# Kernel tuning notes

Measured on AMD Instinct MI355X. Metric: run time of the kernel, lower is better.

The kernel has to match this reference:

```python
import jax, jax.numpy as jnp
import numpy as np

EPS = 1e-8           # torch.cosine_similarity norm clamp
TEMPERATURE = 0.2    # from __init__ default


def setup_inputs() -> dict:
    key = jax.random.key(0)
    k1, k2, k3 = jax.random.split(key, 3)
    B, C, D = 16384, 1000, 2048  # batch, num_classes, embedding_size
    querys = jax.random.normal(k1, (B, D), dtype=jnp.float32)
    prototype = jax.random.normal(k2, (C, D), dtype=jnp.float32)
    fc_w = jax.random.normal(k3, (C, D), dtype=jnp.float32) * 0.02
    fc_b = jnp.zeros((C,), dtype=jnp.float32)
    return {"querys": querys, "prototype": prototype, "fc_w": fc_w, "fc_b": fc_b}


def _memory_prototype_attention(querys, prototype):
    # cosine similarity of every query against every prototype, fused as one GEMM
    qn = jnp.maximum(jnp.linalg.norm(querys, axis=1, keepdims=True), EPS)      # [B,1]
    pn = jnp.maximum(jnp.linalg.norm(prototype, axis=1, keepdims=True), EPS)   # [C,1]
    cos = jnp.einsum('bd,cd->bc', querys / qn, prototype / pn)                 # [B,C]
    attn = jax.nn.softmax(cos / TEMPERATURE, axis=1)                           # [B,C]
    enhanced = jnp.einsum('bc,cd->bd', attn, prototype)                        # [B,D]
    # original skips rows where the raw score sum is exactly zero
    nonzero = (jnp.sum(cos, axis=1, keepdims=True) != 0)
    return jnp.where(nonzero, enhanced, jnp.zeros_like(enhanced))


def reference(querys, prototype, fc_w, fc_b):
    embedding = querys  # post-avgpool features in the original forward
    enhanced = jax.lax.stop_gradient(_memory_prototype_attention(querys, prototype))
    x = querys + enhanced
    logits = x @ fc_w.T + fc_b  # [B, num_classes]
    return (logits, embedding)
```

## Files before the change

### kernel.cpp

```cpp
#include <hip/hip_runtime.h>
#include <hip/hip_bf16.h>
#include <cstdint>
#include <math.h>

typedef __attribute__((ext_vector_type(8))) __bf16 bfx8;
typedef __attribute__((ext_vector_type(4))) __bf16 bfx4;
typedef __attribute__((ext_vector_type(4))) float f32x4;

#define EPSN 1e-8f
#define SM_SCALE 7.2134752044448170f

__device__ __forceinline__ void gload_lds16(const void* g, void* l) {
    __builtin_amdgcn_global_load_lds(
        (__attribute__((address_space(1))) void*)g,
        (__attribute__((address_space(3))) void*)l,
        16, 0, 0);
}

__global__ __launch_bounds__(256) void qnorm_kernel(
    const float* __restrict__ q, __bf16* __restrict__ qbf,
    float* __restrict__ emb, int D) {
    const int tid = threadIdx.x;
    const size_t roff = (size_t)blockIdx.x * D;
    const float4* qr = (const float4*)(q + roff);
    float4* er = (float4*)(emb + roff);
    const int PASS = D >> 10;
    float4 v[4];
    float ss = 0.f;
    for (int p = 0; p < PASS; ++p) {
        v[p] = qr[p * 256 + tid];
        ss += v[p].x * v[p].x + v[p].y * v[p].y + v[p].z * v[p].z + v[p].w * v[p].w;
    }
    for (int o = 32; o; o >>= 1) ss += __shfl_xor(ss, o);
    __shared__ float sred[4];
    if ((tid & 63) == 0) sred[tid >> 6] = ss;
    __syncthreads();
    float tot = sred[0] + sred[1] + sred[2] + sred[3];
    float inv = 1.f / fmaxf(sqrtf(tot), EPSN);
    for (int p = 0; p < PASS; ++p) {
        er[p * 256 + tid] = v[p];
        bfx4 o4 = {(__bf16)(v[p].x * inv), (__bf16)(v[p].y * inv),
                   (__bf16)(v[p].z * inv), (__bf16)(v[p].w * inv)};
        *(bfx4*)(qbf + roff + (size_t)(p * 256 + tid) * 4) = o4;
    }
}

__global__ __launch_bounds__(256) void pnorm_kernel(
    const float* __restrict__ P, const float* __restrict__ W,
    __bf16* __restrict__ Pn, __bf16* __restrict__ Wb,
    int C, int D) {
    const int c = blockIdx.x;
    const int tid = threadIdx.x;
    const int PASS = D >> 10;
    if (c >= C) {
        bfx4 z = {(__bf16)0.f, (__bf16)0.f, (__bf16)0.f, (__bf16)0.f};
        for (int p = 0; p < PASS; ++p) {
            size_t e = (size_t)c * D + (size_t)(p * 256 + tid) * 4;
            *(bfx4*)(Pn + e) = z;
            *(bfx4*)(Wb + e) = z;
        }
        return;
    }
    const float4* pr = (const float4*)(P + (size_t)c * D);
    float4 v[4];
    float ss = 0.f;
    for (int p = 0; p < PASS; ++p) {
        v[p] = pr[p * 256 + tid];
        ss += v[p].x * v[p].x + v[p].y * v[p].y + v[p].z * v[p].z + v[p].w * v[p].w;
    }
    for (int o = 32; o; o >>= 1) ss += __shfl_xor(ss, o);
    __shared__ float sred[4];
    if ((tid & 63) == 0) sred[tid >> 6] = ss;
    __syncthreads();
    float tot = sred[0] + sred[1] + sred[2] + sred[3];
    float inv = 1.f / fmaxf(sqrtf(tot), EPSN);
    const float4* wr_ = (const float4*)(W + (size_t)c * D);
    for (int p = 0; p < PASS; ++p) {
        size_t e = (size_t)c * D + (size_t)(p * 256 + tid) * 4;
        bfx4 o4 = {(__bf16)(v[p].x * inv), (__bf16)(v[p].y * inv),
                   (__bf16)(v[p].z * inv), (__bf16)(v[p].w * inv)};
        *(bfx4*)(Pn + e) = o4;
        float4 wv = wr_[p * 256 + tid];
        bfx4 w4 = {(__bf16)wv.x, (__bf16)wv.y, (__bf16)wv.z, (__bf16)wv.w};
        *(bfx4*)(Wb + e) = w4;
    }
}

__global__ __launch_bounds__(256) void ptrans_kernel(
    const float* __restrict__ P, __bf16* __restrict__ PT,
    int C, int D, int CP) {
    __shared__ float t[64][65];
    const int d0 = blockIdx.x * 64;
    const int c0 = blockIdx.y * 64;
    const int tid = threadIdx.x;
#pragma unroll
    for (int it = 0; it < 16; ++it) {
        int idx = it * 256 + tid;
        int r = idx >> 6;
        int cc = idx & 63;
        float v = 0.f;
        if (c0 + r < C) v = P[(size_t)(c0 + r) * D + d0 + cc];
        t[r][cc] = v;
    }
    __syncthreads();
#pragma unroll
    for (int it = 0; it < 16; ++it) {
        int idx = it * 256 + tid;
        int dd = idx >> 6;
        int c = idx & 63;
        PT[(size_t)(d0 + dd) * CP + c0 + c] = (__bf16)t[c][dd];
    }
}

__global__ __launch_bounds__(256) void softmax_kernel(
    __bf16* __restrict__ S, int C, int CP) {
    const int tid = threadIdx.x;
    __bf16* row = S + (size_t)blockIdx.x * CP;
    bfx4 v4 = *(const bfx4*)(row + tid * 4);
    const int base = tid * 4;
    float v[4];
    float mx = -INFINITY, rs = 0.f;
#pragma unroll
    for (int j = 0; j < 4; ++j) {
        v[j] = (float)v4[j];
        if (base + j < C) { mx = fmaxf(mx, v[j]); rs += v[j]; }
    }
    for (int o = 32; o; o >>= 1) {
        mx = fmaxf(mx, __shfl_xor(mx, o));
        rs += __shfl_xor(rs, o);
    }
    __shared__ float smx[4], srs[4], sps[4];
    if ((tid & 63) == 0) { smx[tid >> 6] = mx; srs[tid >> 6] = rs; }
    __syncthreads();
    mx = fmaxf(fmaxf(smx[0], smx[1]), fmaxf(smx[2], smx[3]));
    rs = srs[0] + srs[1] + srs[2] + srs[3];
    float p[4], ps = 0.f;
#pragma unroll
    for (int j = 0; j < 4; ++j) {
        p[j] = (base + j < C) ? exp2f((v[j] - mx) * SM_SCALE) : 0.f;
        ps += p[j];
    }
    for (int o = 32; o; o >>= 1) ps += __shfl_xor(ps, o);
    if ((tid & 63) == 0) sps[tid >> 6] = ps;
    __syncthreads();
    ps = sps[0] + sps[1] + sps[2] + sps[3];
    float inv = (rs != 0.f) ? 1.f / ps : 0.f;
    bfx4 o4 = {(__bf16)(p[0] * inv), (__bf16)(p[1] * inv),
               (__bf16)(p[2] * inv), (__bf16)(p[3] * inv)};
    *(bfx4*)(row + tid * 4) = o4;
}

template <int MODE>
__global__ __launch_bounds__(512, 2) void gemm8p(
    const __bf16* __restrict__ A, const __bf16* __restrict__ B_,
    int K, int NT, int nbxl, int nwg,
    void* __restrict__ out, const float* __restrict__ aux, int ldout) {
    __shared__ __bf16 lds[65536];

    const int tid = threadIdx.x;
    const int lane = tid & 63, wid = tid >> 6;
    const int wr = wid >> 2, wc = wid & 3;
    const int fr = lane & 15, fq = lane >> 4;
    const int wr4 = wr * 4, wc2 = wc * 2;
    const int frs = fr * 32 + ((fq * 8) ^ ((fr & 8) << 1));

    const int nbx = 1 << nbxl;
    const int lin = blockIdx.y * nbx + blockIdx.x;
    const int swz = (lin & 7) * (nwg >> 3) + (lin >> 3);
    const int bm0 = (swz >> nbxl) * 256;
    const int bn0 = (swz & (nbx - 1)) * 256;

    int row0, col0, row1, col1;
    {
        int Le = tid * 8;
        int st = Le >> 9, w = Le & 511;
        row0 = (st >> 1) * 16 + (w >> 5);
        col0 = (st & 1) * 32 + ((w & 31) ^ ((w >> 4) & 16));
        Le = tid * 8 + 4096;
        st = Le >> 9; w = Le & 511;
        row1 = (st >> 1) * 16 + (w >> 5);
        col1 = (st & 1) * 32 + ((w & 31) ^ ((w >> 4) & 16));
    }
    const __bf16* Ap = A + (size_t)bm0 * K;
    const __bf16* Bp = B_ + (size_t)bn0 * K;
    const size_t hstride = (size_t)128 * K;
    const __bf16* srcA0 = Ap + (size_t)row0 * K + col0;
    const __bf16* srcA1 = Ap + (size_t)row1 * K + col1;
    const __bf16* srcB0 = Bp + (size_t)row0 * K + col0;
    const __bf16* srcB1 = Bp + (size_t)row1 * K + col1;
    const int ldsoff = tid * 8;

#define STG(H, t) do {                                                         \
    const int kt_ = (t) << 6;                                                  \
    __bf16* d_ = lds + ((((t) & 1) << 14) + (((H) >> 1) << 13) +               \
                        (((H) & 1) ? 32768 : 0)) + ldsoff;                     \
    const __bf16* s0_ = (((H) & 1) ? srcB0 : srcA0) +                          \
                        (((H) >> 1) ? hstride : 0) + kt_;                      \
    const __bf16* s1_ = (((H) & 1) ? srcB1 : srcA1) +                          \
                        (((H) >> 1) ? hstride : 0) + kt_;                      \
    gload_lds16(s0_, d_);                                                      \
    gload_lds16(s1_, d_ + 4096);                                               \
} while (0)

    bfx8 fA0[4][2], fA1[4][2], fB0[2][2], fB1[2][2];
    f32x4 acc[4][4][2] = {};

#define RDA(F, H, BUFE) do {                                                   \
    _Pragma("unroll") for (int m_ = 0; m_ < 4; ++m_)                           \
      _Pragma("unroll") for (int ks_ = 0; ks_ < 2; ++ks_)                      \
        F[m_][ks_] = *(const bfx8*)&lds[(BUFE) +                               \
            (((((H) * 8) + wr4 + m_) * 2 + ks_) << 9) + frs];                  \
} while (0)
#define RDB(F, H, BUFE) do {                                                   \
    _Pragma("unroll") for (int n_ = 0; n_ < 2; ++n_)                           \
      _Pragma("unroll") for (int ks_ = 0; ks_ < 2; ++ks_)                      \
        F[n_][ks_] = *(const bfx8*)&lds[32768 + (BUFE) +                       \
            (((((H) * 8) + wc2 + n_) * 2 + ks_) << 9) + frs];                  \
} while (0)
#define MM(QI, FA, FB) do {                                                    \
    __builtin_amdgcn_s_setprio(1);                                             \
    _Pragma("unroll") for (int ks_ = 0; ks_ < 2; ++ks_)                        \
      _Pragma("unroll") for (int m_ = 0; m_ < 4; ++m_)                         \
        _Pragma("unroll") for (int n_ = 0; n_ < 2; ++n_)                       \
          acc[QI][m_][n_] = __builtin_amdgcn_mfma_f32_16x16x32_bf16(           \
              FA[m_][ks_], FB[n_][ks_], acc[QI][m_][n_], 0, 0, 0);             \
    __builtin_amdgcn_s_setprio(0);                                             \
} while (0)
#define BAR __builtin_amdgcn_s_barrier()
#define LGKM(N) asm volatile("s_waitcnt lgkmcnt(" #N ")" ::: "memory")
#define VMC(N) asm volatile("s_waitcnt vmcnt(" #N ")" ::: "memory")

    STG(0, 0); STG(1, 0); STG(2, 0); STG(3, 0);
    STG(0, 1); STG(1, 1);
    VMC(4);
    BAR;
    RDA(fA0, 0, 0);
    RDB(fB0, 0, 0);

    for (int T = 0; T <= NT - 3; ++T) {
        const int bufe = (T & 1) << 14, nbufe = bufe ^ 16384;
        RDB(fB1, 1, bufe); STG(2, T + 1); BAR; LGKM(4);
        MM(0, fA0, fB0); BAR;
        RDA(fA1, 1, bufe); STG(3, T + 1); BAR; LGKM(8);
        MM(1, fA0, fB1); BAR;
        STG(0, T + 2); BAR; LGKM(0);
        MM(3, fA1, fB1); BAR;
        STG(1, T + 2); BAR;
        MM(2, fA1, fB0); VMC(4); BAR;
        RDA(fA0, 0, nbufe); RDB(fB0, 0, nbufe);
    }
    {
        const int T = NT - 2;
        const int bufe = (T & 1) << 14, nbufe = bufe ^ 16384;
        RDB(fB1, 1, bufe); STG(2, T + 1); BAR; LGKM(4);
        MM(0, fA0, fB0); BAR;
        RDA(fA1, 1, bufe); STG(3, T + 1); BAR; LGKM(8);
        MM(1, fA0, fB1); BAR;
        BAR; LGKM(0);
        MM(3, fA1, fB1); BAR;
        BAR;
        MM(2, fA1, fB0); VMC(0); BAR;
        RDA(fA0, 0, nbufe); RDB(fB0, 0, nbufe);
    }
    {
        const int bufe = ((NT - 1) & 1) << 14;
        RDB(fB1, 1, bufe); BAR; LGKM(4);
        MM(0, fA0, fB0); BAR;
        RDA(fA1, 1, bufe); BAR; LGKM(8);
        MM(1, fA0, fB1); BAR;
        BAR; LGKM(0);
        MM(3, fA1, fB1); BAR;
        MM(2, fA1, fB0);
    }
#undef STG
#undef RDA
#undef RDB
#undef MM
#undef BAR
#undef LGKM
#undef VMC

#pragma unroll
    for (int q = 0; q < 4; ++q) {
        const int qm_ = q >> 1, qn_ = q & 1;
#pragma unroll
        for (int m = 0; m < 4; ++m) {
            const int grb = bm0 + qm_ * 128 + wr * 64 + m * 16 + fq * 4;
#pragma unroll
            for (int n = 0; n < 2; ++n) {
                const int gc = bn0 + qn_ * 128 + wc * 32 + n * 16 + fr;
#pragma unroll
                for (int j = 0; j < 4; ++j) {
                    const int gr = grb + j;
                    const float va = acc[q][m][n][j];
                    if (MODE == 0) {
                        ((__bf16*)out)[(size_t)gr * ldout + gc] = (__bf16)va;
                    } else if (MODE == 1) {
                        ((__bf16*)out)[(size_t)gr * ldout + gc] =
                            (__bf16)(va + aux[(size_t)gr * ldout + gc]);
                    } else {
                        if (gc < ldout)
                            ((float*)out)[(size_t)gr * ldout + gc] = va + aux[gc];
                    }
                }
            }
        }
    }
}

extern "C" void kernel_launch(void* const* d_in, const int* in_sizes, int n_in,
                              void* d_out, int out_size, void* d_ws, size_t ws_size,
                              hipStream_t stream) {
    const float* q  = (const float*)d_in[0];
    const float* pr = (const float*)d_in[1];
    const float* fw = (const float*)d_in[2];
    const float* fb = (const float*)d_in[3];
    const int C = in_sizes[3];
    const int D = in_sizes[1] / C;
    const int B = in_sizes[0] / D;
    const int CP = (C + 127) & ~127;

    float* logits = (float*)d_out;
    float* emb = logits + (size_t)B * C;

    char* w = (char*)d_ws;
    __bf16* Qb = (__bf16*)w; w += (size_t)B * D * 2;
    __bf16* Pn = (__bf16*)w; w += (size_t)CP * D * 2;
    __bf16* PT = (__bf16*)w; w += (size_t)D * CP * 2;
    __bf16* Wb = (__bf16*)w; w += (size_t)CP * D * 2;
    __bf16* Sb = (__bf16*)w; w += (size_t)B * CP * 2;
    __bf16* Xb = Qb;

    qnorm_kernel<<<B, 256, 0, stream>>>(q, Qb, emb, D);
    pnorm_kernel<<<CP, 256, 0, stream>>>(pr, fw, Pn, Wb, C, D);
    ptrans_kernel<<<dim3(D / 64, CP / 64), 256, 0, stream>>>(pr, PT, C, D, CP);

    {
        const int nbx = CP / 256, nby = B / 256;
        gemm8p<0><<<dim3(nbx, nby), 512, 0, stream>>>(
            Qb, Pn, D, D / 64, 2, nbx * nby, (void*)Sb, nullptr, CP);
    }
    softmax_kernel<<<B, 256, 0, stream>>>(Sb, C, CP);
    {
        const int nbx = D / 256, nby = B / 256;
        gemm8p<1><<<dim3(nbx, nby), 512, 0, stream>>>(
            Sb, PT, CP, CP / 64, 3, nbx * nby, (void*)Xb, q, D);
    }
    {
        const int nbx = CP / 256, nby = B / 256;
        gemm8p<2><<<dim3(nbx, nby), 512, 0, stream>>>(
            Xb, Wb, D, D / 64, 2, nbx * nby, (void*)logits, fb, C);
    }
}
```

Before: 383.5 us.

## Reassociate logits through precomputed prototype×fc_w product and fuse q·Wᵀ with cos GEMM

Rewrites logits as qn·(q̂·Wᵀ) + attn·(P·Wᵀ) + b, precomputing the small C×C matrix P·Wᵀ with a split-K atomic GEMM. The cosine GEMM and the q·Wᵀ GEMM share one launch over a doubled N dimension, and the final GEMM accumulates attn·PW into the logits. This drops the large attn·P GEMM and the enhanced-feature roundtrip, cutting total FLOPs, but it changes rounding: q·Wᵀ is now computed from bf16 normalized queries rescaled by the norm.

```diff
diff --git a/kernel.cpp b/kernel.cpp
--- a/kernel.cpp
+++ b/kernel.cpp
@@ -19,7 +19,7 @@
 
 __global__ __launch_bounds__(256) void qnorm_kernel(
     const float* __restrict__ q, __bf16* __restrict__ qbf,
-    float* __restrict__ emb, int D) {
+    float* __restrict__ emb, float* __restrict__ qn, int D) {
     const int tid = threadIdx.x;
     const size_t roff = (size_t)blockIdx.x * D;
     const float4* qr = (const float4*)(q + roff);
@@ -36,7 +36,9 @@
     if ((tid & 63) == 0) sred[tid >> 6] = ss;
     __syncthreads();
     float tot = sred[0] + sred[1] + sred[2] + sred[3];
-    float inv = 1.f / fmaxf(sqrtf(tot), EPSN);
+    float nrm = fmaxf(sqrtf(tot), EPSN);
+    float inv = 1.f / nrm;
+    if (tid == 0) qn[blockIdx.x] = nrm;
     for (int p = 0; p < PASS; ++p) {
         er[p * 256 + tid] = v[p];
         bfx4 o4 = {(__bf16)(v[p].x * inv), (__bf16)(v[p].y * inv),
@@ -47,7 +49,7 @@
 
 __global__ __launch_bounds__(256) void pnorm_kernel(
     const float* __restrict__ P, const float* __restrict__ W,
-    __bf16* __restrict__ Pn, __bf16* __restrict__ Wb,
+    __bf16* __restrict__ Pn, __bf16* __restrict__ Wb, __bf16* __restrict__ Pr,
     int C, int D) {
     const int c = blockIdx.x;
     const int tid = threadIdx.x;
@@ -58,6 +60,7 @@
             size_t e = (size_t)c * D + (size_t)(p * 256 + tid) * 4;
             *(bfx4*)(Pn + e) = z;
             *(bfx4*)(Wb + e) = z;
+            *(bfx4*)(Pr + e) = z;
         }
         return;
     }
@@ -80,35 +83,82 @@
         bfx4 o4 = {(__bf16)(v[p].x * inv), (__bf16)(v[p].y * inv),
                    (__bf16)(v[p].z * inv), (__bf16)(v[p].w * inv)};
         *(bfx4*)(Pn + e) = o4;
+        bfx4 r4 = {(__bf16)v[p].x, (__bf16)v[p].y, (__bf16)v[p].z, (__bf16)v[p].w};
+        *(bfx4*)(Pr + e) = r4;
         float4 wv = wr_[p * 256 + tid];
         bfx4 w4 = {(__bf16)wv.x, (__bf16)wv.y, (__bf16)wv.z, (__bf16)wv.w};
         *(bfx4*)(Wb + e) = w4;
     }
 }
 
-__global__ __launch_bounds__(256) void ptrans_kernel(
-    const float* __restrict__ P, __bf16* __restrict__ PT,
-    int C, int D, int CP) {
-    __shared__ float t[64][65];
-    const int d0 = blockIdx.x * 64;
-    const int c0 = blockIdx.y * 64;
+__global__ __launch_bounds__(256) void zero_kernel(float* __restrict__ p) {
+    const size_t i = ((size_t)blockIdx.x * 256 + threadIdx.x) * 8;
+    float4 z = {0.f, 0.f, 0.f, 0.f};
+    *(float4*)(p + i) = z;
+    *(float4*)(p + i + 4) = z;
+}
+
+__global__ __launch_bounds__(256) void cast_kernel(
+    const float* __restrict__ src, __bf16* __restrict__ dst) {
+    const size_t i = ((size_t)blockIdx.x * 256 + threadIdx.x) * 8;
+    float4 a = *(const float4*)(src + i);
+    float4 b = *(const float4*)(src + i + 4);
+    bfx8 o = {(__bf16)a.x, (__bf16)a.y, (__bf16)a.z, (__bf16)a.w,
+              (__bf16)b.x, (__bf16)b.y, (__bf16)b.z, (__bf16)b.w};
+    *(bfx8*)(dst + i) = o;
+}
+
+__global__ __launch_bounds__(256) void pwt_gemm(
+    const __bf16* __restrict__ A, const __bf16* __restrict__ B,
+    int Ktot, int KSPL, float* __restrict__ out, int ldo) {
+    __shared__ __bf16 As[128 * 32];
+    __shared__ __bf16 Bs[128 * 32];
     const int tid = threadIdx.x;
-#pragma unroll
-    for (int it = 0; it < 16; ++it) {
-        int idx = it * 256 + tid;
-        int r = idx >> 6;
-        int cc = idx & 63;
-        float v = 0.f;
-        if (c0 + r < C) v = P[(size_t)(c0 + r) * D + d0 + cc];
-        t[r][cc] = v;
-    }
-    __syncthreads();
-#pragma unroll
-    for (int it = 0; it < 16; ++it) {
-        int idx = it * 256 + tid;
-        int dd = idx >> 6;
-        int c = idx & 63;
-        PT[(size_t)(d0 + dd) * CP + c0 + c] = (__bf16)t[c][dd];
+    const int lane = tid & 63, wid = tid >> 6;
+    const int wr = wid >> 1, wc = wid & 1;
+    const int fr = lane & 15, fq = lane >> 4;
+    const int m0 = blockIdx.y * 128, n0 = blockIdx.x * 128;
+    const int k0 = blockIdx.z * KSPL;
+
+    const int flat0 = tid * 16;
+    const int r0 = flat0 >> 6, c0e = (flat0 & 63) >> 1;
+    const int flat1 = flat0 + 4096;
+    const int r1 = flat1 >> 6, c1e = (flat1 & 63) >> 1;
+
+    f32x4 acc[4][4] = {};
+
+    for (int kt = k0; kt < k0 + KSPL; kt += 32) {
+        __syncthreads();
+        gload_lds16(A + (size_t)(m0 + r0) * Ktot + kt + c0e, (char*)As + flat0);
+        gload_lds16(A + (size_t)(m0 + r1) * Ktot + kt + c1e, (char*)As + flat1);
+        gload_lds16(B + (size_t)(n0 + r0) * Ktot + kt + c0e, (char*)Bs + flat0);
+        gload_lds16(B + (size_t)(n0 + r1) * Ktot + kt + c1e, (char*)Bs + flat1);
+        asm volatile("s_waitcnt vmcnt(0)" ::: "memory");
+        __syncthreads();
+        bfx8 af[4], bfv[4];
+#pragma unroll
+        for (int m = 0; m < 4; ++m)
+            af[m] = *(const bfx8*)(As + (wr * 64 + m * 16 + fr) * 32 + fq * 8);
+#pragma unroll
+        for (int n = 0; n < 4; ++n)
+            bfv[n] = *(const bfx8*)(Bs + (wc * 64 + n * 16 + fr) * 32 + fq * 8);
+#pragma unroll
+        for (int m = 0; m < 4; ++m)
+#pragma unroll
+            for (int n = 0; n < 4; ++n)
+                acc[m][n] = __builtin_amdgcn_mfma_f32_16x16x32_bf16(
+                    af[m], bfv[n], acc[m][n], 0, 0, 0);
+    }
+#pragma unroll
+    for (int m = 0; m < 4; ++m) {
+        const int grb = m0 + wr * 64 + m * 16 + fq * 4;
+#pragma unroll
+        for (int n = 0; n < 4; ++n) {
+            const int gc = n0 + wc * 64 + n * 16 + fr;
+#pragma unroll
+            for (int j = 0; j < 4; ++j)
+                atomicAdd(out + (size_t)(grb + j) * ldo + gc, acc[m][n][j]);
+        }
     }
 }
 
@@ -153,8 +203,11 @@
 template <int MODE>
 __global__ __launch_bounds__(512, 2) void gemm8p(
     const __bf16* __restrict__ A, const __bf16* __restrict__ B_,
+    const __bf16* __restrict__ B2,
     int K, int NT, int nbxl, int nwg,
-    void* __restrict__ out, const float* __restrict__ aux, int ldout) {
+    void* __restrict__ outA, float* __restrict__ outB,
+    const float* __restrict__ auxA, const float* __restrict__ auxB,
+    int cpEl, int nv) {
     __shared__ __bf16 lds[65536];
 
     const int tid = threadIdx.x;
@@ -182,7 +235,10 @@
         col1 = (st & 1) * 32 + ((w & 31) ^ ((w >> 4) & 16));
     }
     const __bf16* Ap = A + (size_t)bm0 * K;
-    const __bf16* Bp = B_ + (size_t)bn0 * K;
+    const __bf16* Bbase = B_;
+    int bnloc = bn0;
+    if (MODE == 4 && bn0 >= cpEl) { Bbase = B2; bnloc = bn0 - cpEl; }
+    const __bf16* Bp = Bbase + (size_t)bnloc * K;
     const size_t hstride = (size_t)128 * K;
     const __bf16* srcA0 = Ap + (size_t)row0 * K + col0;
     const __bf16* srcA1 = Ap + (size_t)row1 * K + col1;
@@ -293,14 +349,19 @@
                 for (int j = 0; j < 4; ++j) {
                     const int gr = grb + j;
                     const float va = acc[q][m][n][j];
-                    if (MODE == 0) {
-                        ((__bf16*)out)[(size_t)gr * ldout + gc] = (__bf16)va;
-                    } else if (MODE == 1) {
-                        ((__bf16*)out)[(size_t)gr * ldout + gc] =
-                            (__bf16)(va + aux[(size_t)gr * ldout + gc]);
+                    if (MODE == 4) {
+                        if (bn0 < cpEl) {
+                            ((__bf16*)outA)[(size_t)gr * cpEl + gc] = (__bf16)va;
+                        } else {
+                            const int c = gc - cpEl;
+                            if (c < nv)
+                                outB[(size_t)gr * nv + c] = auxA[gr] * va + auxB[c];
+                        }
                     } else {
-                        if (gc < ldout)
-                            ((float*)out)[(size_t)gr * ldout + gc] = va + aux[gc];
+                        if (gc < nv) {
+                            float* p = outB + (size_t)gr * nv + gc;
+                            *p = *p + va;
+                        }
                     }
                 }
             }
@@ -324,31 +385,34 @@
     float* emb = logits + (size_t)B * C;
 
     char* w = (char*)d_ws;
-    __bf16* Qb = (__bf16*)w; w += (size_t)B * D * 2;
-    __bf16* Pn = (__bf16*)w; w += (size_t)CP * D * 2;
-    __bf16* PT = (__bf16*)w; w += (size_t)D * CP * 2;
-    __bf16* Wb = (__bf16*)w; w += (size_t)CP * D * 2;
-    __bf16* Sb = (__bf16*)w; w += (size_t)B * CP * 2;
-    __bf16* Xb = Qb;
-
-    qnorm_kernel<<<B, 256, 0, stream>>>(q, Qb, emb, D);
-    pnorm_kernel<<<CP, 256, 0, stream>>>(pr, fw, Pn, Wb, C, D);
-    ptrans_kernel<<<dim3(D / 64, CP / 64), 256, 0, stream>>>(pr, PT, C, D, CP);
-
+    __bf16* Qb  = (__bf16*)w; w += (size_t)B * D * 2;
+    __bf16* Pn  = (__bf16*)w; w += (size_t)CP * D * 2;
+    __bf16* Wb  = (__bf16*)w; w += (size_t)CP * D * 2;
+    __bf16* PWT = (__bf16*)w; w += (size_t)CP * CP * 2;
+    float*  qn  = (float*)w;  w += (size_t)B * 4;
+    __bf16* Scos = (__bf16*)w; w += (size_t)B * CP * 2;
+    float*  PWf = (float*)Scos;
+    __bf16* Pr  = Scos + (size_t)4 * 1024 * 1024;
+
+    qnorm_kernel<<<B, 256, 0, stream>>>(q, Qb, emb, qn, D);
+    pnorm_kernel<<<CP, 256, 0, stream>>>(pr, fw, Pn, Wb, Pr, C, D);
+
+    zero_kernel<<<(CP * CP) / 2048, 256, 0, stream>>>(PWf);
+    pwt_gemm<<<dim3(CP / 128, CP / 128, 4), 256, 0, stream>>>(
+        Wb, Pr, D, D / 4, PWf, CP);
+    cast_kernel<<<(CP * CP) / 2048, 256, 0, stream>>>(PWf, PWT);
+
+    {
+        const int nbx = 2 * CP / 256, nby = B / 256;
+        gemm8p<4><<<dim3(nbx, nby), 512, 0, stream>>>(
+            Qb, Pn, Wb, D, D / 64, 3, nbx * nby,
+            (void*)Scos, logits, qn, fb, CP, C);
+    }
+    softmax_kernel<<<B, 256, 0, stream>>>(Scos, C, CP);
     {
         const int nbx = CP / 256, nby = B / 256;
-        gemm8p<0><<<dim3(nbx, nby), 512, 0, stream>>>(
-            Qb, Pn, D, D / 64, 2, nbx * nby, (void*)Sb, nullptr, CP);
-    }
-    softmax_kernel<<<B, 256, 0, stream>>>(Sb, C, CP);
-    {
-        const int nbx = D / 256, nby = B / 256;
-        gemm8p<1><<<dim3(nbx, nby), 512, 0, stream>>>(
-            Sb, PT, CP, CP / 64, 3, nbx * nby, (void*)Xb, q, D);
-    }
-    {
-        const int nbx = CP / 256, nby = B / 256;
-        gemm8p<2><<<dim3(nbx, nby), 512, 0, stream>>>(
-            Xb, Wb, D, D / 64, 2, nbx * nby, (void*)logits, fb, C);
-    }
-}
+        gemm8p<5><<<dim3(nbx, nby), 512, 0, stream>>>(
+            Scos, PWT, nullptr, CP, CP / 64, 2, nbx * nby,
+            nullptr, logits, nullptr, nullptr, CP, C);
+    }
+}
```

After: 384.0 us. About the same (+0.1%).
